# Kernel tuning notes

Hardware: AMD Instinct MI355X
Metric: run time of the kernel (lower is better)

The kernel has to match this reference:

```python
import jax, jax.numpy as jnp
from jax import lax
import numpy as np

B, CIN, COUT, WDIM, RES = 8, 512, 512, 512, 64


def setup_inputs() -> dict:
    key = jax.random.key(0)
    k0, k1, k2, k3 = jax.random.split(key, 4)
    x = jax.random.normal(k0, (B, CIN, RES, RES), dtype=jnp.float32)
    w = jax.random.normal(k1, (B, WDIM), dtype=jnp.float32)
    weight = jax.random.normal(k2, (COUT, CIN, 3, 3), dtype=jnp.float32)
    bias = jnp.zeros((COUT,), dtype=jnp.float32)
    affine_w = jax.random.normal(k3, (CIN, WDIM), dtype=jnp.float32) * 0.02
    affine_b = jnp.zeros((CIN,), dtype=jnp.float32)
    return {"x": x, "w": w, "weight": weight, "bias": bias,
            "affine_w": affine_w, "affine_b": affine_b}


def reference(x, w, weight, bias, affine_w, affine_b):
    # style: [B, Cin] = affine(w)
    style = w @ affine_w.T + affine_b
    b, cin, h, wd = x.shape
    cout = weight.shape[0]
    # per-sample modulated weight: [B, Cout, Cin, 3, 3]
    wmod = weight[None, :, :, :, :] * style[:, None, :, None, None]
    # grouped conv with groups = batch: lhs [1, B*Cin, H, W], rhs [B*Cout, Cin, 3, 3]
    lhs = x.reshape(1, b * cin, h, wd)
    rhs = wmod.reshape(b * cout, cin, 3, 3)
    y = lax.conv_general_dilated(
        lhs, rhs,
        window_strides=(1, 1),
        padding=[(1, 1), (1, 1)],
        dimension_numbers=("NCHW", "OIHW", "NCHW"),
        feature_group_count=b,
    )
    y = y.reshape(b, cout, h, wd)
    return y + bias[None, :, None, None]
```

## Files before the change

kernel.cpp:

```cpp
#include <hip/hip_runtime.h>
#include <cstdint>
#include <cstddef>

#define BATCH 8
#define CIN   512
#define COUT  512
#define RES   64
#define HW    4096
#define WDIM  512

typedef short bf16x8 __attribute__((ext_vector_type(8)));
typedef float f32x4  __attribute__((ext_vector_type(4)));
typedef float f32x4v __attribute__((ext_vector_type(4)));
typedef unsigned short ushort8 __attribute__((ext_vector_type(8)));

typedef const __attribute__((address_space(1))) void* gas_ptr;
typedef __attribute__((address_space(3))) void*       las_ptr;

__device__ __forceinline__ unsigned short f2bf(float f) {
    unsigned int u = __float_as_uint(f);
    u += 0x7fffu + ((u >> 16) & 1u);
    return (unsigned short)(u >> 16);
}

__global__ __launch_bounds__(256) void prep_kernel(
    const float* __restrict__ x,  const float* __restrict__ w,
    const float* __restrict__ aw, const float* __restrict__ ab,
    const float* __restrict__ wt,
    unsigned short* __restrict__ xs, unsigned short* __restrict__ wr,
    unsigned short* __restrict__ zpage)
{
    __shared__ float sh[4608];
    const int bid = blockIdx.x;
    const int t   = threadIdx.x;

    if (bid < 512) {
        const int b   = bid & 7;
        const int ci0 = ((bid >> 3) & 7) * 64;
        const int hwb = (bid >> 6) * 512;

        float* tile     = sh;
        float* partials = sh + 4160;
        float* styleS   = sh + 4416;

        {
            int cil = t >> 2, q = t & 3;
            const f32x4v* arow = (const f32x4v*)(aw + (size_t)(ci0 + cil) * WDIM + q * 128);
            const f32x4v* wrow = (const f32x4v*)(w + (size_t)b * WDIM + q * 128);
            float s = 0.f;
#pragma unroll
            for (int i = 0; i < 32; ++i) {
                f32x4v a = arow[i], ww = wrow[i];
                s += a.x * ww.x + a.y * ww.y + a.z * ww.z + a.w * ww.w;
            }
            partials[t] = s;
        }
        __syncthreads();
        if (t < 64)
            styleS[t] = partials[t * 4] + partials[t * 4 + 1] + partials[t * 4 + 2]
                      + partials[t * 4 + 3] + ab[ci0 + t];
        __syncthreads();

        int sub = t >> 6, lane = t & 63;
        int ci8 = (t & 7) * 8;
        for (int tl = 0; tl < 8; ++tl) {
            int hw0 = hwb + tl * 64;
#pragma unroll
            for (int r = 0; r < 16; ++r) {
                int ci = r * 4 + sub;
                tile[ci * 65 + lane] =
                    x[((size_t)(b * CIN + ci0 + ci)) * HW + hw0 + lane] * styleS[ci];
            }
            __syncthreads();
#pragma unroll
            for (int r = 0; r < 2; ++r) {
                int hw = r * 32 + (t >> 3);
                ushort8 v;
#pragma unroll
                for (int j = 0; j < 8; ++j) v[j] = f2bf(tile[(ci8 + j) * 65 + hw]);
                *(ushort8*)&xs[((size_t)b * HW + hw0 + hw) * CIN + ci0 + ci8] = v;
            }
            __syncthreads();
        }
    } else {
        if (bid == 512 && t < 128) zpage[t] = 0;
        int co = bid - 512;
#pragma unroll
        for (int r = 0; r < 18; ++r) sh[r * 256 + t] = wt[(size_t)co * 4608 + r * 256 + t];
        __syncthreads();
#pragma unroll
        for (int r = 0; r < 18; ++r) {
            int idx = r * 256 + t;
            int tap = idx >> 9, ci = idx & 511;
            wr[(size_t)tap * (COUT * CIN) + co * CIN + ci] = f2bf(sh[ci * 9 + tap]);
        }
    }
}

__global__ __launch_bounds__(512) void conv_kernel(
    const unsigned short* __restrict__ xs,
    const unsigned short* __restrict__ wr,
    const float* __restrict__ bias,
    const unsigned short* __restrict__ zpage,
    float* __restrict__ y)
{
    __shared__ __align__(16) unsigned short As[3 * 128 * 32];
    __shared__ __align__(16) unsigned short Bs[4 * 66 * 32];

    const int t   = threadIdx.x;
    const int bid = blockIdx.x;
    const int b   = bid & 7;
    const int h0  = ((bid >> 3) & 15) * 4;
    const int co0 = (bid >> 7) * 128;

    const int lane = t & 63;
    const int wv   = t >> 6;
    const int wm   = (wv & 1) * 64;
    const int wn   = (wv >> 1) * 64;
    const int r16  = lane & 15;
    const int quad = lane >> 4;

    if (t < 256) {
        int s = t >> 6, c = t & 63;
        int col = (c < 32) ? 0 : 65;
        Bs[(s * 66 + col) * 32 + (c & 31)] = 0;
    }

    f32x4 acc[4][4];
#pragma unroll
    for (int mi = 0; mi < 4; ++mi)
#pragma unroll
        for (int ni = 0; ni < 4; ++ni)
            acc[mi][ni] = (f32x4){0.f, 0.f, 0.f, 0.f};

    for (int kh = 0; kh < 3; ++kh) {
        const unsigned short* pA[3];
#pragma unroll
        for (int L = 0; L < 3; ++L) {
            int lin = L * 512 + t;
            int tap = kh * 3 + (lin >> 9);
            int q   = (lin >> 2) & 127;
            int c8  = ((lin & 3) ^ ((lin >> 3) & 3)) * 8;
            pA[L] = wr + (size_t)tap * (COUT * CIN) + (co0 + q) * CIN + c8;
        }
        const unsigned short* pB[2];
        int sB[2];
#pragma unroll
        for (int L = 0; L < 2; ++L) {
            int lin = L * 512 + t;
            int s  = lin >> 8, r8 = lin & 255;
            int wc = r8 >> 2;
            int rowp = s * 66 + 1 + wc;
            int c8 = ((r8 & 3) ^ ((rowp >> 1) & 3)) * 8;
            int hp = h0 + kh - 1 + s;
            bool ok = (unsigned)hp < 64u;
            pB[L] = ok ? xs + ((size_t)b * HW + hp * 64 + wc) * CIN + c8 : zpage;
            sB[L] = ok ? 32 : 0;
        }

        for (int ch = 0; ch < 16; ++ch) {
#pragma unroll
            for (int L = 0; L < 3; ++L) {
                int lin = L * 512 + t;
                __builtin_amdgcn_global_load_lds((gas_ptr)pA[L], (las_ptr)&As[lin * 8], 16, 0, 0);
                pA[L] += 32;
            }
#pragma unroll
            for (int L = 0; L < 2; ++L) {
                int lin = L * 512 + t;
                int s = lin >> 8, r8 = lin & 255;
                __builtin_amdgcn_global_load_lds((gas_ptr)pB[L],
                    (las_ptr)&Bs[(s * 66 + 1) * 32 + r8 * 8], 16, 0, 0);
                pB[L] += sB[L];
            }
            __syncthreads();
#pragma unroll
            for (int kw = 0; kw < 3; ++kw) {
                bf16x8 af[4], bfv[4];
#pragma unroll
                for (int mi = 0; mi < 4; ++mi) {
                    int row = kw * 128 + wm + mi * 16 + r16;
                    int ck  = quad ^ ((row >> 1) & 3);
                    af[mi] = *(const bf16x8*)&As[row * 32 + ck * 8];
                }
#pragma unroll
                for (int ni = 0; ni < 4; ++ni) {
                    int n = wn + ni * 16 + r16;
                    int dh = n >> 6, wc = n & 63;
                    int row = dh * 66 + wc + kw;
                    int ck  = quad ^ ((row >> 1) & 3);
                    bfv[ni] = *(const bf16x8*)&Bs[row * 32 + ck * 8];
                }
#pragma unroll
                for (int mi = 0; mi < 4; ++mi)
#pragma unroll
                    for (int ni = 0; ni < 4; ++ni)
                        acc[mi][ni] = __builtin_amdgcn_mfma_f32_16x16x32_bf16(
                            af[mi], bfv[ni], acc[mi][ni], 0, 0, 0);
            }
            __syncthreads();
        }
    }

#pragma unroll
    for (int mi = 0; mi < 4; ++mi) {
#pragma unroll
        for (int r = 0; r < 4; ++r) {
            int m = co0 + wm + mi * 16 + quad * 4 + r;
            float bv = bias[m];
            size_t base = ((size_t)b * COUT + m) * HW + h0 * 64;
#pragma unroll
            for (int ni = 0; ni < 4; ++ni) {
                int n = wn + ni * 16 + r16;
                y[base + n] = acc[mi][ni][r] + bv;
            }
        }
    }
}

extern "C" void kernel_launch(void* const* d_in, const int* in_sizes, int n_in,
                              void* d_out, int out_size, void* d_ws, size_t ws_size,
                              hipStream_t stream)
{
    (void)in_sizes; (void)n_in; (void)out_size; (void)ws_size;
    const float* x    = (const float*)d_in[0];
    const float* w    = (const float*)d_in[1];
    const float* wt   = (const float*)d_in[2];
    const float* bias = (const float*)d_in[3];
    const float* aw   = (const float*)d_in[4];
    const float* ab   = (const float*)d_in[5];
    float* y = (float*)d_out;

    char* ws = (char*)d_ws;
    unsigned short* zpage = (unsigned short*)(ws + 16384);
    unsigned short* wr    = (unsigned short*)(ws + 32768);
    unsigned short* xs    = (unsigned short*)(ws + 4751360);

    prep_kernel<<<1024, 256, 0, stream>>>(x, w, aw, ab, wt, xs, wr, zpage);
    conv_kernel<<<512, 512, 0, stream>>>(xs, wr, bias, zpage, y);
}
```

Baseline: 272.4 us.

## Load conv weights directly from global memory and widen input K-chunk staging

The conv kernel stops staging weight tiles in LDS and has each lane read its A fragments straight from global memory (relying on caches). The input tile is staged in 64-channel chunks with an 8-way XOR swizzle, halving the number of barrier-separated iterations, and launch bounds request 4 waves per SIMD. The prep kernel is split into 8x more blocks, each handling one 64-pixel tile instead of looping over 8. The trade-off is that weight fragments are now re-fetched from global/L2 by every block and wave, with their latency sitting directly in the MFMA loop instead of being shared through LDS.

Result: slower. 575.9 us (+111.4%).

```diff
diff --git a/kernel.cpp b/kernel.cpp
--- a/kernel.cpp
+++ b/kernel.cpp
@@ -11,7 +11,6 @@
 
 typedef short bf16x8 __attribute__((ext_vector_type(8)));
 typedef float f32x4  __attribute__((ext_vector_type(4)));
-typedef float f32x4v __attribute__((ext_vector_type(4)));
 typedef unsigned short ushort8 __attribute__((ext_vector_type(8)));
 
 typedef const __attribute__((address_space(1))) void* gas_ptr;
@@ -34,10 +33,10 @@
     const int bid = blockIdx.x;
     const int t   = threadIdx.x;
 
-    if (bid < 512) {
+    if (bid < 4096) {
         const int b   = bid & 7;
         const int ci0 = ((bid >> 3) & 7) * 64;
-        const int hwb = (bid >> 6) * 512;
+        const int hw0 = (bid >> 6) * 64;
 
         float* tile     = sh;
         float* partials = sh + 4160;
@@ -45,12 +44,12 @@
 
         {
             int cil = t >> 2, q = t & 3;
-            const f32x4v* arow = (const f32x4v*)(aw + (size_t)(ci0 + cil) * WDIM + q * 128);
-            const f32x4v* wrow = (const f32x4v*)(w + (size_t)b * WDIM + q * 128);
+            const f32x4* arow = (const f32x4*)(aw + (size_t)(ci0 + cil) * WDIM + q * 128);
+            const f32x4* wrow = (const f32x4*)(w + (size_t)b * WDIM + q * 128);
             float s = 0.f;
 #pragma unroll
             for (int i = 0; i < 32; ++i) {
-                f32x4v a = arow[i], ww = wrow[i];
+                f32x4 a = arow[i], ww = wrow[i];
                 s += a.x * ww.x + a.y * ww.y + a.z * ww.z + a.w * ww.w;
             }
             partials[t] = s;
@@ -62,29 +61,25 @@
         __syncthreads();
 
         int sub = t >> 6, lane = t & 63;
+#pragma unroll
+        for (int r = 0; r < 16; ++r) {
+            int ci = r * 4 + sub;
+            tile[ci * 65 + lane] =
+                x[((size_t)(b * CIN + ci0 + ci)) * HW + hw0 + lane] * styleS[ci];
+        }
+        __syncthreads();
         int ci8 = (t & 7) * 8;
-        for (int tl = 0; tl < 8; ++tl) {
-            int hw0 = hwb + tl * 64;
-#pragma unroll
-            for (int r = 0; r < 16; ++r) {
-                int ci = r * 4 + sub;
-                tile[ci * 65 + lane] =
-                    x[((size_t)(b * CIN + ci0 + ci)) * HW + hw0 + lane] * styleS[ci];
-            }
-            __syncthreads();
-#pragma unroll
-            for (int r = 0; r < 2; ++r) {
-                int hw = r * 32 + (t >> 3);
-                ushort8 v;
-#pragma unroll
-                for (int j = 0; j < 8; ++j) v[j] = f2bf(tile[(ci8 + j) * 65 + hw]);
-                *(ushort8*)&xs[((size_t)b * HW + hw0 + hw) * CIN + ci0 + ci8] = v;
-            }
-            __syncthreads();
+#pragma unroll
+        for (int r = 0; r < 2; ++r) {
+            int hw = r * 32 + (t >> 3);
+            ushort8 v;
+#pragma unroll
+            for (int j = 0; j < 8; ++j) v[j] = f2bf(tile[(ci8 + j) * 65 + hw]);
+            *(ushort8*)&xs[((size_t)b * HW + hw0 + hw) * CIN + ci0 + ci8] = v;
         }
     } else {
-        if (bid == 512 && t < 128) zpage[t] = 0;
-        int co = bid - 512;
+        if (bid == 4096 && t < 128) zpage[t] = 0;
+        int co = bid - 4096;
 #pragma unroll
         for (int r = 0; r < 18; ++r) sh[r * 256 + t] = wt[(size_t)co * 4608 + r * 256 + t];
         __syncthreads();
@@ -97,15 +92,14 @@
     }
 }
 
-__global__ __launch_bounds__(512) void conv_kernel(
+__global__ __launch_bounds__(512, 4) void conv_kernel(
     const unsigned short* __restrict__ xs,
     const unsigned short* __restrict__ wr,
     const float* __restrict__ bias,
     const unsigned short* __restrict__ zpage,
     float* __restrict__ y)
 {
-    __shared__ __align__(16) unsigned short As[3 * 128 * 32];
-    __shared__ __align__(16) unsigned short Bs[4 * 66 * 32];
+    __shared__ __align__(16) unsigned short Bs[4 * 66 * 64];
 
     const int t   = threadIdx.x;
     const int bid = blockIdx.x;
@@ -120,11 +114,16 @@
     const int r16  = lane & 15;
     const int quad = lane >> 4;
 
-    if (t < 256) {
-        int s = t >> 6, c = t & 63;
-        int col = (c < 32) ? 0 : 65;
-        Bs[(s * 66 + col) * 32 + (c & 31)] = 0;
-    }
+    {
+        int s = t >> 7, rest = t & 127;
+        int col = (rest < 64) ? 0 : 65;
+        Bs[(s * 66 + col) * 64 + (rest & 63)] = 0;
+    }
+
+    int avoff[4];
+#pragma unroll
+    for (int mi = 0; mi < 4; ++mi)
+        avoff[mi] = (co0 + wm + mi * 16 + r16) * CIN + quad * 8;
 
     f32x4 acc[4][4];
 #pragma unroll
@@ -134,69 +133,51 @@
             acc[mi][ni] = (f32x4){0.f, 0.f, 0.f, 0.f};
 
     for (int kh = 0; kh < 3; ++kh) {
-        const unsigned short* pA[3];
-#pragma unroll
-        for (int L = 0; L < 3; ++L) {
-            int lin = L * 512 + t;
-            int tap = kh * 3 + (lin >> 9);
-            int q   = (lin >> 2) & 127;
-            int c8  = ((lin & 3) ^ ((lin >> 3) & 3)) * 8;
-            pA[L] = wr + (size_t)tap * (COUT * CIN) + (co0 + q) * CIN + c8;
-        }
-        const unsigned short* pB[2];
-        int sB[2];
-#pragma unroll
-        for (int L = 0; L < 2; ++L) {
-            int lin = L * 512 + t;
-            int s  = lin >> 8, r8 = lin & 255;
-            int wc = r8 >> 2;
-            int rowp = s * 66 + 1 + wc;
-            int c8 = ((r8 & 3) ^ ((rowp >> 1) & 3)) * 8;
-            int hp = h0 + kh - 1 + s;
+        const unsigned short* pB[4];
+        int sB[4];
+#pragma unroll
+        for (int L = 0; L < 4; ++L) {
+            int wc = t >> 3, c = t & 7;
+            int rowp = L * 66 + 1 + wc;
+            int csrc = c ^ (rowp & 7);
+            int hp = h0 + kh - 1 + L;
             bool ok = (unsigned)hp < 64u;
-            pB[L] = ok ? xs + ((size_t)b * HW + hp * 64 + wc) * CIN + c8 : zpage;
-            sB[L] = ok ? 32 : 0;
-        }
-
-        for (int ch = 0; ch < 16; ++ch) {
-#pragma unroll
-            for (int L = 0; L < 3; ++L) {
-                int lin = L * 512 + t;
-                __builtin_amdgcn_global_load_lds((gas_ptr)pA[L], (las_ptr)&As[lin * 8], 16, 0, 0);
-                pA[L] += 32;
-            }
-#pragma unroll
-            for (int L = 0; L < 2; ++L) {
-                int lin = L * 512 + t;
-                int s = lin >> 8, r8 = lin & 255;
+            pB[L] = ok ? xs + ((size_t)b * HW + hp * 64 + wc) * CIN + csrc * 8 : zpage;
+            sB[L] = ok ? 64 : 0;
+        }
+
+        for (int ch = 0; ch < 8; ++ch) {
+#pragma unroll
+            for (int L = 0; L < 4; ++L) {
                 __builtin_amdgcn_global_load_lds((gas_ptr)pB[L],
-                    (las_ptr)&Bs[(s * 66 + 1) * 32 + r8 * 8], 16, 0, 0);
+                    (las_ptr)&Bs[(L * 66 + 1) * 64 + t * 8], 16, 0, 0);
                 pB[L] += sB[L];
             }
             __syncthreads();
 #pragma unroll
             for (int kw = 0; kw < 3; ++kw) {
-                bf16x8 af[4], bfv[4];
-#pragma unroll
-                for (int mi = 0; mi < 4; ++mi) {
-                    int row = kw * 128 + wm + mi * 16 + r16;
-                    int ck  = quad ^ ((row >> 1) & 3);
-                    af[mi] = *(const bf16x8*)&As[row * 32 + ck * 8];
+                const size_t tapoff = (size_t)(kh * 3 + kw) * (COUT * CIN) + ch * 64;
+#pragma unroll
+                for (int ksub = 0; ksub < 2; ++ksub) {
+                    bf16x8 af[4], bfv[4];
+#pragma unroll
+                    for (int mi = 0; mi < 4; ++mi)
+                        af[mi] = *(const bf16x8*)&wr[tapoff + avoff[mi] + ksub * 32];
+#pragma unroll
+                    for (int ni = 0; ni < 4; ++ni) {
+                        int n = wn + ni * 16 + r16;
+                        int dh = n >> 6, wc = n & 63;
+                        int rowp = dh * 66 + wc + kw;
+                        int cph = (ksub * 4 + quad) ^ (rowp & 7);
+                        bfv[ni] = *(const bf16x8*)&Bs[rowp * 64 + cph * 8];
+                    }
+#pragma unroll
+                    for (int mi = 0; mi < 4; ++mi)
+#pragma unroll
+                        for (int ni = 0; ni < 4; ++ni)
+                            acc[mi][ni] = __builtin_amdgcn_mfma_f32_16x16x32_bf16(
+                                af[mi], bfv[ni], acc[mi][ni], 0, 0, 0);
                 }
-#pragma unroll
-                for (int ni = 0; ni < 4; ++ni) {
-                    int n = wn + ni * 16 + r16;
-                    int dh = n >> 6, wc = n & 63;
-                    int row = dh * 66 + wc + kw;
-                    int ck  = quad ^ ((row >> 1) & 3);
-                    bfv[ni] = *(const bf16x8*)&Bs[row * 32 + ck * 8];
-                }
-#pragma unroll
-                for (int mi = 0; mi < 4; ++mi)
-#pragma unroll
-                    for (int ni = 0; ni < 4; ++ni)
-                        acc[mi][ni] = __builtin_amdgcn_mfma_f32_16x16x32_bf16(
-                            af[mi], bfv[ni], acc[mi][ni], 0, 0, 0);
             }
             __syncthreads();
         }
@@ -236,6 +217,6 @@
     unsigned short* wr    = (unsigned short*)(ws + 32768);
     unsigned short* xs    = (unsigned short*)(ws + 4751360);
 
-    prep_kernel<<<1024, 256, 0, stream>>>(x, w, aw, ab, wt, xs, wr, zpage);
+    prep_kernel<<<4608, 256, 0, stream>>>(x, w, aw, ab, wt, xs, wr, zpage);
     conv_kernel<<<512, 512, 0, stream>>>(xs, wr, bias, zpage, y);
 }
```
